# Performance work log

Measured on AMD Instinct MI355X. Metric: run time of the kernel, lower is better.

## Reference

```python
import jax, jax.numpy as jnp
import numpy as np

K, D, B, T = 512, 256, 32, 4096

def setup_inputs() -> dict:
    key = jax.random.key(0)
    k1, k2 = jax.random.split(key)
    z_e_x = jax.random.normal(k1, (B, D, T), dtype=jnp.float32)
    # nn.Embedding weight init uniform(-1/K, 1/K)
    emb_weight = jax.random.uniform(k2, (K, D), dtype=jnp.float32, minval=-1.0 / K, maxval=1.0 / K)
    return {"z_e_x": z_e_x, "emb_weight": emb_weight}

def reference(z_e_x, emb_weight):
    # forward(): permute [B,D,T] -> [B,T,D], nearest-codebook indices
    z = jnp.transpose(z_e_x, (0, 2, 1))  # [B, T, D]
    # squared L2 distances: ||z||^2 - 2 z.W^T + ||W||^2  -> [B, T, K]
    z_sq = jnp.sum(z * z, axis=-1, keepdims=True)           # [B, T, 1]
    w_sq = jnp.sum(emb_weight * emb_weight, axis=-1)        # [K]
    cross = jnp.einsum('btd,kd->btk', z, emb_weight)        # [B, T, K]
    dists = z_sq - 2.0 * cross + w_sq[None, None, :]
    latents = jnp.argmin(dists, axis=-1)                    # [B, T] int
    return latents
```

## Files before the change

kernel.cpp:

```cpp
#include <hip/hip_runtime.h>
#include <math.h>

#define NK 512
#define DD 256
#define NB 32
#define NT 4096

typedef __attribute__((ext_vector_type(8))) _Float16 f16x8;
typedef __attribute__((ext_vector_type(4))) float f32x4;

#define MARGIN 1.5e-4f
#define DCH 16
#define NCH 16
#define KPC 32
#define APAD 40

__device__ __forceinline__ unsigned short f16bits(float x) {
    _Float16 h = (_Float16)x;
    unsigned short s;
    __builtin_memcpy(&s, &h, 2);
    return s;
}

__global__ __launch_bounds__(512) void prep_kernel(const float* __restrict__ W,
                                                   unsigned short* __restrict__ Wpp,
                                                   float* __restrict__ wsq) {
    const int bx = blockIdx.x;
    const int k  = threadIdx.x;
    if (bx < NCH) {
        const int d0 = bx * DCH;
        float w[16];
        const float4* src4 = (const float4*)(W + (size_t)k * DD + d0);
        #pragma unroll
        for (int q = 0; q < 4; ++q) {
            float4 v = src4[q];
            w[4 * q + 0] = v.x; w[4 * q + 1] = v.y; w[4 * q + 2] = v.z; w[4 * q + 3] = v.w;
        }
        __align__(16) unsigned int dw[16];
        #pragma unroll
        for (int j = 0; j < 16; ++j) {
            unsigned short s = f16bits(w[j] * 4096.0f);
            dw[j] = (unsigned int)s | ((unsigned int)s << 16);
        }
        unsigned short* dst = Wpp + ((size_t)bx * 512 + k) * 32;
        #pragma unroll
        for (int j = 0; j < 4; ++j) ((int4*)dst)[j] = ((const int4*)dw)[j];
    } else {
        const float4* row = (const float4*)(W + (size_t)k * DD);
        double s = 0.0;
        #pragma unroll 8
        for (int i = 0; i < DD / 4; ++i) {
            float4 v = row[i];
            s += (double)v.x * v.x + (double)v.y * v.y + (double)v.z * v.z + (double)v.w * v.w;
        }
        wsq[k] = (float)s;
    }
}

__global__ __launch_bounds__(256, 2) void vq_phase1(const float* __restrict__ Z,
                                                    const unsigned short* __restrict__ Wpp,
                                                    const float* __restrict__ wsq,
                                                    float* __restrict__ gq1,
                                                    float* __restrict__ gq2,
                                                    int* __restrict__ gi1) {
    __shared__ __align__(16) short As[128 * APAD];
    __shared__ __align__(16) short Bs[256 * APAD];

    const int tid  = threadIdx.x;
    const int wave = tid >> 6;
    const int lane = tid & 63;
    const int lm   = lane & 15;
    const int lq   = lane >> 4;
    const int mw   = wave & 1;
    const int nw   = wave >> 1;

    const int bx = blockIdx.x;
    const int h  = bx & 1;
    const int tl = bx >> 1;
    const int b  = tl >> 5;
    const int t0 = (tl & 31) * 128;

    const int t_l = tid & 127;
    const int dg  = tid >> 7;

    const float* zcol = Z + (size_t)b * DD * NT + t0 + t_l;

    f32x4 acc[4][8];
    #pragma unroll
    for (int mt = 0; mt < 4; ++mt)
        #pragma unroll
        for (int nt = 0; nt < 8; ++nt)
            acc[mt][nt] = (f32x4){0.f, 0.f, 0.f, 0.f};

    double zacc = 0.0;

    for (int c = 0; c < NCH; ++c) {
        const int d0 = c * DCH;
        __syncthreads();

        {
            float zv[8];
            #pragma unroll
            for (int j = 0; j < 8; ++j)
                zv[j] = zcol[(size_t)(d0 + dg * 8 + j) * NT];
            #pragma unroll
            for (int j = 0; j < 8; ++j)
                zacc = fma((double)zv[j], (double)zv[j], zacc);

            __align__(16) unsigned int u[8];
            #pragma unroll
            for (int j = 0; j < 8; ++j) {
                _Float16 zh = (_Float16)zv[j];
                float rz = zv[j] - (float)zh;
                unsigned short hs, ls;
                __builtin_memcpy(&hs, &zh, 2);
                ls = f16bits(rz);
                u[j] = (unsigned int)hs | ((unsigned int)ls << 16);
            }
            int4* dst = (int4*)&As[t_l * APAD + dg * 16];
            dst[0] = ((const int4*)u)[0];
            dst[1] = ((const int4*)u)[1];
        }
        {
            const unsigned short* src = Wpp + ((size_t)c * 512 + h * 256 + tid) * 32;
            int4 v0 = ((const int4*)src)[0];
            int4 v1 = ((const int4*)src)[1];
            int4 v2 = ((const int4*)src)[2];
            int4 v3 = ((const int4*)src)[3];
            int4* bd = (int4*)&Bs[tid * APAD];
            bd[0] = v0; bd[1] = v1; bd[2] = v2; bd[3] = v3;
        }
        __syncthreads();

        f16x8 a[4], bb[8];
        #pragma unroll
        for (int mt = 0; mt < 4; ++mt)
            a[mt] = *(const f16x8*)&As[(mw * 64 + mt * 16 + lm) * APAD + lq * 8];
        #pragma unroll
        for (int nt = 0; nt < 8; ++nt)
            bb[nt] = *(const f16x8*)&Bs[(nw * 128 + nt * 16 + lm) * APAD + lq * 8];
        #pragma unroll
        for (int mt = 0; mt < 4; ++mt)
            #pragma unroll
            for (int nt = 0; nt < 8; ++nt)
                acc[mt][nt] = __builtin_amdgcn_mfma_f32_16x16x32_f16(
                    a[mt], bb[nt], acc[mt][nt], 0, 0, 0);
    }

    __syncthreads();
    double* zred = (double*)As;
    zred[dg * 128 + t_l] = zacc;
    __syncthreads();
    float* zf = (float*)Bs;
    if (tid < 128) zf[tid] = (float)(zred[tid] + zred[128 + tid]);
    __syncthreads();

    float wq[8];
    #pragma unroll
    for (int nt = 0; nt < 8; ++nt)
        wq[nt] = wsq[h * 256 + nw * 128 + nt * 16 + lm];
    const int kbase = h * 256 + nw * 128 + lm;

    float* cb1 = (float*)As;
    float* cb2 = cb1 + 256;
    int*   cbi = (int*)(cb2 + 256);

    #pragma unroll
    for (int mt = 0; mt < 4; ++mt) {
        #pragma unroll
        for (int r = 0; r < 4; ++r) {
            float zz = zf[mw * 64 + mt * 16 + lq * 4 + r];
            float q1 = INFINITY, q2 = INFINITY;
            int i1 = 0x7fffffff;
            #pragma unroll
            for (int nt = 0; nt < 8; ++nt) {
                float c2   = __fmul_rn(acc[mt][nt][r], 4.8828125e-4f);
                float dist = __fadd_rn(__fsub_rn(zz, c2), wq[nt]);
                int kk = kbase + nt * 16;
                if (dist < q1 || (dist == q1 && kk < i1)) { q2 = q1; q1 = dist; i1 = kk; }
                else if (dist < q2) q2 = dist;
            }
            #pragma unroll
            for (int mk = 1; mk <= 8; mk <<= 1) {
                float o1 = __shfl_xor(q1, mk);
                float o2 = __shfl_xor(q2, mk);
                int   oi = __shfl_xor(i1, mk);
                if (o1 < q1 || (o1 == q1 && oi < i1)) { q2 = fminf(q1, o2); q1 = o1; i1 = oi; }
                else { q2 = fminf(o1, q2); }
            }
            if (lm == 0) {
                int m = mw * 64 + mt * 16 + lq * 4 + r;
                cb1[m * 2 + nw] = q1;
                cb2[m * 2 + nw] = q2;
                cbi[m * 2 + nw] = i1;
            }
        }
    }
    __syncthreads();
    if (tid < 128) {
        float a1 = cb1[tid * 2],     a2 = cb2[tid * 2];     int ai = cbi[tid * 2];
        float b1 = cb1[tid * 2 + 1], b2 = cb2[tid * 2 + 1]; int bi = cbi[tid * 2 + 1];
        float q1, q2; int i1;
        if (b1 < a1 || (b1 == a1 && bi < ai)) { q1 = b1; i1 = bi; q2 = fminf(a1, b2); }
        else { q1 = a1; i1 = ai; q2 = fminf(b1, a2); }
        size_t bt = (size_t)b * NT + t0 + tid;
        gq1[bt * 2 + h] = q1;
        gq2[bt * 2 + h] = q2;
        gi1[bt * 2 + h] = i1;
    }
}

__global__ __launch_bounds__(256) void vq_fixmerge(const float* __restrict__ Z,
                                                   const float* __restrict__ W,
                                                   const float* __restrict__ wsq,
                                                   const float* __restrict__ gq1,
                                                   const float* __restrict__ gq2,
                                                   const int* __restrict__ gi1,
                                                   int* __restrict__ out) {
    __shared__ __align__(16) float Zs[8][256];
    __shared__ double pz[8][32];
    __shared__ float  zsqs[8];
    __shared__ int    bts[8];
    __shared__ float  rv[8][4];
    __shared__ int    ri[8][4];
    __shared__ int    lcnt;
    __shared__ int    llist[256];

    const int tid  = threadIdx.x;
    const int lane = tid & 63;
    const int wv   = tid >> 6;
    const int bt   = blockIdx.x * 256 + tid;

    if (tid == 0) lcnt = 0;
    __syncthreads();

    {
        float a1 = gq1[(size_t)bt * 2],     a2 = gq2[(size_t)bt * 2];     int ai = gi1[(size_t)bt * 2];
        float b1 = gq1[(size_t)bt * 2 + 1], b2 = gq2[(size_t)bt * 2 + 1]; int bi = gi1[(size_t)bt * 2 + 1];
        float q1, q2; int i1;
        if (b1 < a1 || (b1 == a1 && bi < ai)) { q1 = b1; i1 = bi; q2 = fminf(a1, b2); }
        else { q1 = a1; i1 = ai; q2 = fminf(b1, a2); }
        out[bt] = i1;
        if (q2 - q1 <= MARGIN) {
            int p = atomicAdd(&lcnt, 1);
            llist[p] = bt;
        }
    }
    __syncthreads();
    const int n = lcnt;

    for (int base = 0; base < n; base += 8) {
        const int m = (n - base < 8) ? (n - base) : 8;
        __syncthreads();
        if (tid < 8) bts[tid] = llist[base + ((tid < m) ? tid : 0)];
        __syncthreads();

        #pragma unroll
        for (int i = 0; i < 8; ++i) {
            if (i < m) {
                int tb = bts[i];
                int bb = tb >> 12, t = tb & 4095;
                Zs[i][tid] = Z[(size_t)bb * DD * NT + (size_t)tid * NT + t];
            }
        }
        __syncthreads();

        {
            int i = tid >> 5, seg = tid & 31;
            double s = 0.0;
            #pragma unroll
            for (int j = 0; j < 8; ++j) {
                double zz = (double)Zs[i][seg * 8 + j];
                s = fma(zz, zz, s);
            }
            pz[i][seg] = s;
        }
        __syncthreads();
        if (tid < 8) {
            double s = 0.0;
            #pragma unroll
            for (int j = 0; j < 32; ++j) s += pz[tid][j];
            zsqs[tid] = (float)s;
        }
        __syncthreads();

        float da[2][8];
        #pragma unroll
        for (int rr = 0; rr < 2; ++rr) {
            int k = tid + rr * 256;
            const float4* wr = (const float4*)(W + (size_t)k * DD);
            float a8[8];
            #pragma unroll
            for (int i = 0; i < 8; ++i) a8[i] = 0.f;
            for (int q = 0; q < 64; ++q) {
                float4 w4 = wr[q];
                #pragma unroll
                for (int i = 0; i < 8; ++i) {
                    float4 z4 = *(const float4*)&Zs[i][4 * q];
                    a8[i] = fmaf(z4.x, w4.x, a8[i]);
                    a8[i] = fmaf(z4.y, w4.y, a8[i]);
                    a8[i] = fmaf(z4.z, w4.z, a8[i]);
                    a8[i] = fmaf(z4.w, w4.w, a8[i]);
                }
            }
            float wqv = wsq[k];
            #pragma unroll
            for (int i = 0; i < 8; ++i)
                da[rr][i] = __fadd_rn(__fsub_rn(zsqs[i], __fmul_rn(2.0f, a8[i])), wqv);
        }

        #pragma unroll
        for (int i = 0; i < 8; ++i) {
            float v = da[0][i]; int ix = tid;
            if (da[1][i] < v) { v = da[1][i]; ix = tid + 256; }
            #pragma unroll
            for (int mk = 1; mk <= 32; mk <<= 1) {
                float ov = __shfl_xor(v, mk);
                int   oi = __shfl_xor(ix, mk);
                if (ov < v || (ov == v && oi < ix)) { v = ov; ix = oi; }
            }
            if (lane == 0) { rv[i][wv] = v; ri[i][wv] = ix; }
        }
        __syncthreads();
        if (tid < 8 && tid < m) {
            float v = INFINITY; int ix = 0x7fffffff;
            #pragma unroll
            for (int w = 0; w < 4; ++w) {
                if (rv[tid][w] < v || (rv[tid][w] == v && ri[tid][w] < ix)) {
                    v = rv[tid][w]; ix = ri[tid][w];
                }
            }
            out[bts[tid]] = ix;
        }
    }
}

#define BT 128
#define BK 128
#define DCHUNK 32
#define NKC (NK / BK)
#define NDC (DD / DCHUNK)
#define WSTR (BK + 4)

__global__ __launch_bounds__(256) void vq_fallback(const float* __restrict__ Z,
                                                   const float* __restrict__ W,
                                                   int* __restrict__ out) {
    __shared__ __align__(16) float Zs[DCHUNK * BT];
    __shared__ __align__(16) float Ws[DCHUNK * WSTR];
    __shared__ float wsqs[NK];

    const int tid = threadIdx.x;
    const int tx  = tid & 15;
    const int ty  = tid >> 4;
    const int b   = blockIdx.y;
    const int t0  = blockIdx.x * BT;

    for (int k = tid; k < NK; k += 256) {
        const float4* row = (const float4*)(W + (size_t)k * DD);
        double s = 0.0;
        for (int i = 0; i < DD / 4; ++i) {
            float4 v = row[i];
            s += (double)v.x * v.x + (double)v.y * v.y + (double)v.z * v.z + (double)v.w * v.w;
        }
        wsqs[k] = (float)s;
    }

    const float* Zb = Z + (size_t)b * DD * NT + t0;

    float best[8]; int bidx[8];
    #pragma unroll
    for (int a = 0; a < 8; ++a) { best[a] = INFINITY; bidx[a] = 0x7fffffff; }
    double zsqd[8];
    #pragma unroll
    for (int a = 0; a < 8; ++a) zsqd[a] = 0.0;
    float zsqf[8];

    for (int kc = 0; kc < NKC; ++kc) {
        float acc[8][8];
        #pragma unroll
        for (int a = 0; a < 8; ++a)
            #pragma unroll
            for (int c = 0; c < 8; ++c) acc[a][c] = 0.f;

        for (int dc = 0; dc < NDC; ++dc) {
            const int d0 = dc * DCHUNK;
            __syncthreads();
            #pragma unroll
            for (int i = 0; i < 4; ++i) {
                int f  = tid + i * 256;
                int r  = f >> 5;
                int c4 = f & 31;
                float4 v = *(const float4*)(Zb + (size_t)(d0 + r) * NT + c4 * 4);
                *(float4*)(&Zs[r * BT + c4 * 4]) = v;
            }
            #pragma unroll
            for (int i = 0; i < 4; ++i) {
                int u  = tid + i * 256;
                int k  = u >> 3;
                int rg = u & 7;
                float4 v = *(const float4*)(W + (size_t)(kc * BK + k) * DD + d0 + rg * 4);
                Ws[(rg * 4 + 0) * WSTR + k] = v.x;
                Ws[(rg * 4 + 1) * WSTR + k] = v.y;
                Ws[(rg * 4 + 2) * WSTR + k] = v.z;
                Ws[(rg * 4 + 3) * WSTR + k] = v.w;
            }
            __syncthreads();
            #pragma unroll 4
            for (int d = 0; d < DCHUNK; ++d) {
                float4 z0 = *(const float4*)(&Zs[d * BT + ty * 8]);
                float4 z1 = *(const float4*)(&Zs[d * BT + ty * 8 + 4]);
                float4 w0 = *(const float4*)(&Ws[d * WSTR + tx * 8]);
                float4 w1 = *(const float4*)(&Ws[d * WSTR + tx * 8 + 4]);
                float za[8] = {z0.x, z0.y, z0.z, z0.w, z1.x, z1.y, z1.z, z1.w};
                float wa[8] = {w0.x, w0.y, w0.z, w0.w, w1.x, w1.y, w1.z, w1.w};
                if (kc == 0) {
                    #pragma unroll
                    for (int a = 0; a < 8; ++a)
                        zsqd[a] = fma((double)za[a], (double)za[a], zsqd[a]);
                }
                #pragma unroll
                for (int a = 0; a < 8; ++a)
                    #pragma unroll
                    for (int c = 0; c < 8; ++c)
                        acc[a][c] = fmaf(za[a], wa[c], acc[a][c]);
            }
        }
        if (kc == 0) {
            #pragma unroll
            for (int a = 0; a < 8; ++a) zsqf[a] = (float)zsqd[a];
        }
        #pragma unroll
        for (int c = 0; c < 8; ++c) {
            int   kg = kc * BK + tx * 8 + c;
            float wqv = wsqs[kg];
            #pragma unroll
            for (int a = 0; a < 8; ++a) {
                float c2   = __fmul_rn(2.0f, acc[a][c]);
                float s    = __fsub_rn(zsqf[a], c2);
                float dist = __fadd_rn(s, wqv);
                if (dist < best[a] || (dist == best[a] && kg < bidx[a])) {
                    best[a] = dist; bidx[a] = kg;
                }
            }
        }
    }
    __syncthreads();
    float* redv = Zs;
    int*   redi = (int*)Ws;
    #pragma unroll
    for (int a = 0; a < 8; ++a) {
        int tl2 = ty * 8 + a;
        redv[tl2 * 16 + tx] = best[a];
        redi[tl2 * 16 + tx] = bidx[a];
    }
    __syncthreads();
    if (tid < BT) {
        float bv = INFINITY; int bi = 0x7fffffff;
        #pragma unroll
        for (int j = 0; j < 16; ++j) {
            float v = redv[tid * 16 + j];
            int   i = redi[tid * 16 + j];
            if (v < bv || (v == bv && i < bi)) { bv = v; bi = i; }
        }
        out[(size_t)b * NT + t0 + tid] = bi;
    }
}

extern "C" void kernel_launch(void* const* d_in, const int* in_sizes, int n_in,
                              void* d_out, int out_size, void* d_ws, size_t ws_size,
                              hipStream_t stream) {
    const float* Z = (const float*)d_in[0];
    const float* W = (const float*)d_in[1];
    int* out = (int*)d_out;

    const size_t OFF_WSQ = 0;
    const size_t OFF_WPP = 2048;
    const size_t OFF_GQ1 = OFF_WPP + 524288;
    const size_t OFF_GQ2 = OFF_GQ1 + 1048576;
    const size_t OFF_GI1 = OFF_GQ2 + 1048576;
    const size_t NEED    = OFF_GI1 + 1048576;

    if (ws_size >= NEED) {
        float* wsq = (float*)((char*)d_ws + OFF_WSQ);
        unsigned short* wpp = (unsigned short*)((char*)d_ws + OFF_WPP);
        float* gq1 = (float*)((char*)d_ws + OFF_GQ1);
        float* gq2 = (float*)((char*)d_ws + OFF_GQ2);
        int*   gi1 = (int*)((char*)d_ws + OFF_GI1);

        prep_kernel<<<dim3(NCH + 1), dim3(512), 0, stream>>>(W, wpp, wsq);
        vq_phase1<<<dim3(2048), dim3(256), 0, stream>>>(Z, wpp, wsq, gq1, gq2, gi1);
        vq_fixmerge<<<dim3(512), dim3(256), 0, stream>>>(Z, W, wsq, gq1, gq2, gi1, out);
    } else {
        vq_fallback<<<dim3(NT / BT, NB), dim3(256), 0, stream>>>(Z, W, out);
    }
}
```

Baseline: 391.4 us.

## Double-buffer phase1 LDS tiles and split fix pass into global-list merge/fix kernels

The phase-1 GEMM loop now double-buffers the A/B LDS tiles, prefetching the next chunk's Z and codebook into registers while MFMAs run on the current buffer, which drops one barrier per iteration. The combined merge/fix kernel is split into a merge kernel that writes provisional indices and appends ambiguous rows to a global list through an atomic counter, and a fix kernel that grid-strides over that list one row per block. This spreads the exact-recompute work evenly across blocks instead of leaving it concentrated in whichever blocks hold ambiguous rows. In exchange it adds a kernel launch, doubles LDS use (which may lower occupancy), and each fix row rereads W without batching.

```diff
diff --git a/kernel.cpp b/kernel.cpp
--- a/kernel.cpp
+++ b/kernel.cpp
@@ -12,8 +12,9 @@
 #define MARGIN 1.5e-4f
 #define DCH 16
 #define NCH 16
-#define KPC 32
 #define APAD 40
+#define ASZ (128 * APAD)
+#define BSZ (256 * APAD)
 
 __device__ __forceinline__ unsigned short f16bits(float x) {
     _Float16 h = (_Float16)x;
@@ -24,9 +25,11 @@
 
 __global__ __launch_bounds__(512) void prep_kernel(const float* __restrict__ W,
                                                    unsigned short* __restrict__ Wpp,
-                                                   float* __restrict__ wsq) {
+                                                   float* __restrict__ wsq,
+                                                   int* __restrict__ cnt) {
     const int bx = blockIdx.x;
     const int k  = threadIdx.x;
+    if (bx == 0 && k == 0) *cnt = 0;
     if (bx < NCH) {
         const int d0 = bx * DCH;
         float w[16];
@@ -63,8 +66,8 @@
                                                     float* __restrict__ gq1,
                                                     float* __restrict__ gq2,
                                                     int* __restrict__ gi1) {
-    __shared__ __align__(16) short As[128 * APAD];
-    __shared__ __align__(16) short Bs[256 * APAD];
+    __shared__ __align__(16) short As[2 * ASZ];
+    __shared__ __align__(16) short Bs[2 * BSZ];
 
     const int tid  = threadIdx.x;
     const int wave = tid >> 6;
@@ -84,6 +87,7 @@
     const int dg  = tid >> 7;
 
     const float* zcol = Z + (size_t)b * DD * NT + t0 + t_l;
+    const unsigned short* wrow = Wpp + (size_t)(h * 256 + tid) * 32;
 
     f32x4 acc[4][8];
     #pragma unroll
@@ -94,19 +98,69 @@
 
     double zacc = 0.0;
 
+    {
+        float zv[8];
+        #pragma unroll
+        for (int j = 0; j < 8; ++j)
+            zv[j] = zcol[(size_t)(dg * 8 + j) * NT];
+        #pragma unroll
+        for (int j = 0; j < 8; ++j)
+            zacc = fma((double)zv[j], (double)zv[j], zacc);
+        __align__(16) unsigned int u[8];
+        #pragma unroll
+        for (int j = 0; j < 8; ++j) {
+            _Float16 zh = (_Float16)zv[j];
+            float rz = zv[j] - (float)zh;
+            unsigned short hs, ls;
+            __builtin_memcpy(&hs, &zh, 2);
+            ls = f16bits(rz);
+            u[j] = (unsigned int)hs | ((unsigned int)ls << 16);
+        }
+        int4* dst = (int4*)&As[t_l * APAD + dg * 16];
+        dst[0] = ((const int4*)u)[0];
+        dst[1] = ((const int4*)u)[1];
+
+        const int4* src = (const int4*)wrow;
+        int4* bd = (int4*)&Bs[tid * APAD];
+        bd[0] = src[0]; bd[1] = src[1]; bd[2] = src[2]; bd[3] = src[3];
+    }
+
     for (int c = 0; c < NCH; ++c) {
-        const int d0 = c * DCH;
+        const int cur = c & 1;
+        const int nxt = cur ^ 1;
         __syncthreads();
 
+        float zv[8];
+        int4 bv[4];
+        if (c + 1 < NCH) {
+            const int d0n = (c + 1) * DCH;
+            #pragma unroll
+            for (int j = 0; j < 8; ++j)
+                zv[j] = zcol[(size_t)(d0n + dg * 8 + j) * NT];
+            const int4* src = (const int4*)(wrow + (size_t)(c + 1) * 512 * 32);
+            bv[0] = src[0]; bv[1] = src[1]; bv[2] = src[2]; bv[3] = src[3];
+        }
+
         {
-            float zv[8];
-            #pragma unroll
-            for (int j = 0; j < 8; ++j)
-                zv[j] = zcol[(size_t)(d0 + dg * 8 + j) * NT];
+            f16x8 a[4], bb[8];
+            #pragma unroll
+            for (int mt = 0; mt < 4; ++mt)
+                a[mt] = *(const f16x8*)&As[cur * ASZ + (mw * 64 + mt * 16 + lm) * APAD + lq * 8];
+            #pragma unroll
+            for (int nt = 0; nt < 8; ++nt)
+                bb[nt] = *(const f16x8*)&Bs[cur * BSZ + (nw * 128 + nt * 16 + lm) * APAD + lq * 8];
+            #pragma unroll
+            for (int mt = 0; mt < 4; ++mt)
+                #pragma unroll
+                for (int nt = 0; nt < 8; ++nt)
+                    acc[mt][nt] = __builtin_amdgcn_mfma_f32_16x16x32_f16(
+                        a[mt], bb[nt], acc[mt][nt], 0, 0, 0);
+        }
+
+        if (c + 1 < NCH) {
             #pragma unroll
             for (int j = 0; j < 8; ++j)
                 zacc = fma((double)zv[j], (double)zv[j], zacc);
-
             __align__(16) unsigned int u[8];
             #pragma unroll
             for (int j = 0; j < 8; ++j) {
@@ -117,34 +171,12 @@
                 ls = f16bits(rz);
                 u[j] = (unsigned int)hs | ((unsigned int)ls << 16);
             }
-            int4* dst = (int4*)&As[t_l * APAD + dg * 16];
+            int4* dst = (int4*)&As[nxt * ASZ + t_l * APAD + dg * 16];
             dst[0] = ((const int4*)u)[0];
             dst[1] = ((const int4*)u)[1];
-        }
-        {
-            const unsigned short* src = Wpp + ((size_t)c * 512 + h * 256 + tid) * 32;
-            int4 v0 = ((const int4*)src)[0];
-            int4 v1 = ((const int4*)src)[1];
-            int4 v2 = ((const int4*)src)[2];
-            int4 v3 = ((const int4*)src)[3];
-            int4* bd = (int4*)&Bs[tid * APAD];
-            bd[0] = v0; bd[1] = v1; bd[2] = v2; bd[3] = v3;
-        }
-        __syncthreads();
-
-        f16x8 a[4], bb[8];
-        #pragma unroll
-        for (int mt = 0; mt < 4; ++mt)
-            a[mt] = *(const f16x8*)&As[(mw * 64 + mt * 16 + lm) * APAD + lq * 8];
-        #pragma unroll
-        for (int nt = 0; nt < 8; ++nt)
-            bb[nt] = *(const f16x8*)&Bs[(nw * 128 + nt * 16 + lm) * APAD + lq * 8];
-        #pragma unroll
-        for (int mt = 0; mt < 4; ++mt)
-            #pragma unroll
-            for (int nt = 0; nt < 8; ++nt)
-                acc[mt][nt] = __builtin_amdgcn_mfma_f32_16x16x32_f16(
-                    a[mt], bb[nt], acc[mt][nt], 0, 0, 0);
+            int4* bd = (int4*)&Bs[nxt * BSZ + tid * APAD];
+            bd[0] = bv[0]; bd[1] = bv[1]; bd[2] = bv[2]; bd[3] = bv[3];
+        }
     }
 
     __syncthreads();
@@ -210,127 +242,101 @@
     }
 }
 
-__global__ __launch_bounds__(256) void vq_fixmerge(const float* __restrict__ Z,
-                                                   const float* __restrict__ W,
-                                                   const float* __restrict__ wsq,
-                                                   const float* __restrict__ gq1,
-                                                   const float* __restrict__ gq2,
-                                                   const int* __restrict__ gi1,
-                                                   int* __restrict__ out) {
-    __shared__ __align__(16) float Zs[8][256];
-    __shared__ double pz[8][32];
-    __shared__ float  zsqs[8];
-    __shared__ int    bts[8];
-    __shared__ float  rv[8][4];
-    __shared__ int    ri[8][4];
-    __shared__ int    lcnt;
-    __shared__ int    llist[256];
+__global__ __launch_bounds__(256) void vq_merge(const float* __restrict__ gq1,
+                                                const float* __restrict__ gq2,
+                                                const int* __restrict__ gi1,
+                                                int* __restrict__ out,
+                                                int* __restrict__ list,
+                                                int* __restrict__ cnt) {
+    const int bt = blockIdx.x * 256 + threadIdx.x;
+    float a1 = gq1[(size_t)bt * 2],     a2 = gq2[(size_t)bt * 2];     int ai = gi1[(size_t)bt * 2];
+    float b1 = gq1[(size_t)bt * 2 + 1], b2 = gq2[(size_t)bt * 2 + 1]; int bi = gi1[(size_t)bt * 2 + 1];
+    float q1, q2; int i1;
+    if (b1 < a1 || (b1 == a1 && bi < ai)) { q1 = b1; i1 = bi; q2 = fminf(a1, b2); }
+    else { q1 = a1; i1 = ai; q2 = fminf(b1, a2); }
+    out[bt] = i1;
+    if (q2 - q1 <= MARGIN) {
+        int idx = atomicAdd(cnt, 1);
+        list[idx] = bt;
+    }
+}
+
+__global__ __launch_bounds__(256) void vq_fix(const float* __restrict__ Z,
+                                              const float* __restrict__ W,
+                                              const float* __restrict__ wsq,
+                                              const int* __restrict__ list,
+                                              const int* __restrict__ cnt,
+                                              int* __restrict__ out) {
+    __shared__ __align__(16) float Zs[256];
+    __shared__ double pz[32];
+    __shared__ float zsq_s;
+    __shared__ float rv[4];
+    __shared__ int   ri[4];
 
     const int tid  = threadIdx.x;
     const int lane = tid & 63;
     const int wv   = tid >> 6;
-    const int bt   = blockIdx.x * 256 + tid;
-
-    if (tid == 0) lcnt = 0;
-    __syncthreads();
-
-    {
-        float a1 = gq1[(size_t)bt * 2],     a2 = gq2[(size_t)bt * 2];     int ai = gi1[(size_t)bt * 2];
-        float b1 = gq1[(size_t)bt * 2 + 1], b2 = gq2[(size_t)bt * 2 + 1]; int bi = gi1[(size_t)bt * 2 + 1];
-        float q1, q2; int i1;
-        if (b1 < a1 || (b1 == a1 && bi < ai)) { q1 = b1; i1 = bi; q2 = fminf(a1, b2); }
-        else { q1 = a1; i1 = ai; q2 = fminf(b1, a2); }
-        out[bt] = i1;
-        if (q2 - q1 <= MARGIN) {
-            int p = atomicAdd(&lcnt, 1);
-            llist[p] = bt;
-        }
-    }
-    __syncthreads();
-    const int n = lcnt;
-
-    for (int base = 0; base < n; base += 8) {
-        const int m = (n - base < 8) ? (n - base) : 8;
+    const int n    = *cnt;
+
+    for (int it = blockIdx.x; it < n; it += gridDim.x) {
         __syncthreads();
-        if (tid < 8) bts[tid] = llist[base + ((tid < m) ? tid : 0)];
+        const int bt = list[it];
+        const int bb = bt >> 12, t = bt & 4095;
+        Zs[tid] = Z[(size_t)bb * DD * NT + (size_t)tid * NT + t];
         __syncthreads();
 
-        #pragma unroll
-        for (int i = 0; i < 8; ++i) {
-            if (i < m) {
-                int tb = bts[i];
-                int bb = tb >> 12, t = tb & 4095;
-                Zs[i][tid] = Z[(size_t)bb * DD * NT + (size_t)tid * NT + t];
-            }
+        if (tid < 32) {
+            double s = 0.0;
+            #pragma unroll
+            for (int j = 0; j < 8; ++j) {
+                double zz = (double)Zs[tid * 8 + j];
+                s = fma(zz, zz, s);
+            }
+            pz[tid] = s;
         }
         __syncthreads();
-
-        {
-            int i = tid >> 5, seg = tid & 31;
+        if (tid == 0) {
             double s = 0.0;
             #pragma unroll
-            for (int j = 0; j < 8; ++j) {
-                double zz = (double)Zs[i][seg * 8 + j];
-                s = fma(zz, zz, s);
-            }
-            pz[i][seg] = s;
+            for (int j = 0; j < 32; ++j) s += pz[j];
+            zsq_s = (float)s;
         }
         __syncthreads();
-        if (tid < 8) {
-            double s = 0.0;
-            #pragma unroll
-            for (int j = 0; j < 32; ++j) s += pz[tid][j];
-            zsqs[tid] = (float)s;
-        }
+
+        const float4* w0 = (const float4*)(W + (size_t)tid * DD);
+        const float4* w1 = (const float4*)(W + (size_t)(tid + 256) * DD);
+        float a0 = 0.f, a1 = 0.f;
+        #pragma unroll 8
+        for (int q = 0; q < 64; ++q) {
+            float4 x = w0[q];
+            float4 y = w1[q];
+            float4 z4 = *(const float4*)&Zs[4 * q];
+            a0 = fmaf(z4.x, x.x, a0); a0 = fmaf(z4.y, x.y, a0);
+            a0 = fmaf(z4.z, x.z, a0); a0 = fmaf(z4.w, x.w, a0);
+            a1 = fmaf(z4.x, y.x, a1); a1 = fmaf(z4.y, y.y, a1);
+            a1 = fmaf(z4.z, y.z, a1); a1 = fmaf(z4.w, y.w, a1);
+        }
+        float zsf = zsq_s;
+        float d0 = __fadd_rn(__fsub_rn(zsf, __fmul_rn(2.0f, a0)), wsq[tid]);
+        float d1 = __fadd_rn(__fsub_rn(zsf, __fmul_rn(2.0f, a1)), wsq[tid + 256]);
+
+        float v = d0; int ix = tid;
+        if (d1 < v) { v = d1; ix = tid + 256; }
+        #pragma unroll
+        for (int mk = 1; mk <= 32; mk <<= 1) {
+            float ov = __shfl_xor(v, mk);
+            int   oi = __shfl_xor(ix, mk);
+            if (ov < v || (ov == v && oi < ix)) { v = ov; ix = oi; }
+        }
+        if (lane == 0) { rv[wv] = v; ri[wv] = ix; }
         __syncthreads();
-
-        float da[2][8];
-        #pragma unroll
-        for (int rr = 0; rr < 2; ++rr) {
-            int k = tid + rr * 256;
-            const float4* wr = (const float4*)(W + (size_t)k * DD);
-            float a8[8];
-            #pragma unroll
-            for (int i = 0; i < 8; ++i) a8[i] = 0.f;
-            for (int q = 0; q < 64; ++q) {
-                float4 w4 = wr[q];
-                #pragma unroll
-                for (int i = 0; i < 8; ++i) {
-                    float4 z4 = *(const float4*)&Zs[i][4 * q];
-                    a8[i] = fmaf(z4.x, w4.x, a8[i]);
-                    a8[i] = fmaf(z4.y, w4.y, a8[i]);
-                    a8[i] = fmaf(z4.z, w4.z, a8[i]);
-                    a8[i] = fmaf(z4.w, w4.w, a8[i]);
-                }
-            }
-            float wqv = wsq[k];
-            #pragma unroll
-            for (int i = 0; i < 8; ++i)
-                da[rr][i] = __fadd_rn(__fsub_rn(zsqs[i], __fmul_rn(2.0f, a8[i])), wqv);
-        }
-
-        #pragma unroll
-        for (int i = 0; i < 8; ++i) {
-            float v = da[0][i]; int ix = tid;
-            if (da[1][i] < v) { v = da[1][i]; ix = tid + 256; }
-            #pragma unroll
-            for (int mk = 1; mk <= 32; mk <<= 1) {
-                float ov = __shfl_xor(v, mk);
-                int   oi = __shfl_xor(ix, mk);
-                if (ov < v || (ov == v && oi < ix)) { v = ov; ix = oi; }
-            }
-            if (lane == 0) { rv[i][wv] = v; ri[i][wv] = ix; }
-        }
-        __syncthreads();
-        if (tid < 8 && tid < m) {
-            float v = INFINITY; int ix = 0x7fffffff;
-            #pragma unroll
-            for (int w = 0; w < 4; ++w) {
-                if (rv[tid][w] < v || (rv[tid][w] == v && ri[tid][w] < ix)) {
-                    v = rv[tid][w]; ix = ri[tid][w];
-                }
-            }
-            out[bts[tid]] = ix;
+        if (tid == 0) {
+            float bv = rv[0]; int bi = ri[0];
+            #pragma unroll
+            for (int w = 1; w < 4; ++w) {
+                if (rv[w] < bv || (rv[w] == bv && ri[w] < bi)) { bv = rv[w]; bi = ri[w]; }
+            }
+            out[bt] = bi;
         }
     }
 }
@@ -473,23 +479,28 @@
     const float* W = (const float*)d_in[1];
     int* out = (int*)d_out;
 
-    const size_t OFF_WSQ = 0;
-    const size_t OFF_WPP = 2048;
-    const size_t OFF_GQ1 = OFF_WPP + 524288;
-    const size_t OFF_GQ2 = OFF_GQ1 + 1048576;
-    const size_t OFF_GI1 = OFF_GQ2 + 1048576;
-    const size_t NEED    = OFF_GI1 + 1048576;
+    const size_t OFF_WSQ  = 0;
+    const size_t OFF_CNT  = 2048;
+    const size_t OFF_LIST = 4096;
+    const size_t OFF_WPP  = OFF_LIST + 524288;
+    const size_t OFF_GQ1  = OFF_WPP + 524288;
+    const size_t OFF_GQ2  = OFF_GQ1 + 1048576;
+    const size_t OFF_GI1  = OFF_GQ2 + 1048576;
+    const size_t NEED     = OFF_GI1 + 1048576;
 
     if (ws_size >= NEED) {
         float* wsq = (float*)((char*)d_ws + OFF_WSQ);
+        int*   cnt = (int*)((char*)d_ws + OFF_CNT);
+        int*   list = (int*)((char*)d_ws + OFF_LIST);
         unsigned short* wpp = (unsigned short*)((char*)d_ws + OFF_WPP);
         float* gq1 = (float*)((char*)d_ws + OFF_GQ1);
         float* gq2 = (float*)((char*)d_ws + OFF_GQ2);
         int*   gi1 = (int*)((char*)d_ws + OFF_GI1);
 
-        prep_kernel<<<dim3(NCH + 1), dim3(512), 0, stream>>>(W, wpp, wsq);
+        prep_kernel<<<dim3(NCH + 1), dim3(512), 0, stream>>>(W, wpp, wsq, cnt);
         vq_phase1<<<dim3(2048), dim3(256), 0, stream>>>(Z, wpp, wsq, gq1, gq2, gi1);
-        vq_fixmerge<<<dim3(512), dim3(256), 0, stream>>>(Z, W, wsq, gq1, gq2, gi1, out);
+        vq_merge<<<dim3(512), dim3(256), 0, stream>>>(gq1, gq2, gi1, out, list, cnt);
+        vq_fix<<<dim3(512), dim3(256), 0, stream>>>(Z, W, wsq, list, cnt, out);
     } else {
         vq_fallback<<<dim3(NT / BT, NB), dim3(256), 0, stream>>>(Z, W, out);
     }
```

After: 435.0 us. 11.2% more time.
